# Performance work log

Measured on AMD Instinct MI355X. Metric: run time of the kernel, lower is better.

Reference implementation:

```python
import jax, jax.numpy as jnp
import numpy as np

B, N, C, H = 4, 1024, 1024, 16
HD = C // H


def setup_inputs() -> dict:
    key = jax.random.key(0)
    ks = jax.random.split(key, 9)
    s = 0.02
    return {
        "x": jax.random.normal(ks[0], (B, N, C), dtype=jnp.float32),
        "qkv_w": jax.random.normal(ks[1], (3 * C, C), dtype=jnp.float32) * s,
        "qkv_b": jax.random.normal(ks[2], (3 * C,), dtype=jnp.float32) * s,
        "proj_w": jax.random.normal(ks[3], (C, C), dtype=jnp.float32) * s,
        "proj_b": jax.random.normal(ks[4], (C,), dtype=jnp.float32) * s,
        "wl": jax.random.normal(ks[5], (H, H), dtype=jnp.float32) * s,
        "bl": jax.random.normal(ks[6], (H,), dtype=jnp.float32) * s,
        "ww": jax.random.normal(ks[7], (H, H), dtype=jnp.float32) * s,
        "bw": jax.random.normal(ks[8], (H,), dtype=jnp.float32) * s,
    }


def reference(x, qkv_w, qkv_b, proj_w, proj_b, wl, bl, ww, bw):
    # qkv: torch Linear convention y = x @ W.T + b
    scale = HD ** (-0.5)
    qkv = (jnp.einsum("bnc,oc->bno", x, qkv_w) + qkv_b)
    qkv = qkv.reshape(B, N, 3, H, HD).transpose(2, 0, 3, 1, 4)  # [3,B,H,N,HD]
    q, k, v = qkv[0] * scale, qkv[1], qkv[2]
    attn = jnp.einsum("bhnd,bhmd->bhnm", q, k)  # [B,H,N,N]
    # talking-heads mix before softmax (proj_l over head dim)
    attn = jnp.einsum("bhnm,gh->bgnm", attn, wl) + bl[:, None, None]
    attn = jax.nn.softmax(attn, axis=-1)
    # talking-heads mix after softmax (proj_w over head dim)
    attn = jnp.einsum("bhnm,gh->bgnm", attn, ww) + bw[:, None, None]
    out = jnp.einsum("bhnm,bhmd->bhnd", attn, v)  # [B,H,N,HD]
    out = out.transpose(0, 2, 1, 3).reshape(B, N, C)
    out = jnp.einsum("bnc,oc->bno", out, proj_w) + proj_b
    return out, attn
```

## Files before the change

kernel.cpp:

```cpp
#include <hip/hip_runtime.h>
#include <hip/hip_bf16.h>

typedef unsigned short u16;
typedef __attribute__((ext_vector_type(8))) __bf16 bf16x8;
typedef __attribute__((ext_vector_type(4))) float f32x4;

#define LDSS 40

__device__ __forceinline__ float bf2f(u16 u) {
    unsigned int x = ((unsigned int)u) << 16;
    return __builtin_bit_cast(float, x);
}
__device__ __forceinline__ u16 f2bf(float f) {
    unsigned int x = __builtin_bit_cast(unsigned int, f);
    unsigned int lsb = (x >> 16) & 1u;
    x += 0x7fffu + lsb;
    return (u16)(x >> 16);
}
__device__ __forceinline__ float bf2f_lo(unsigned int u) { return __builtin_bit_cast(float, u << 16); }
__device__ __forceinline__ float bf2f_hi(unsigned int u) { return __builtin_bit_cast(float, u & 0xffff0000u); }

__device__ __forceinline__ void ld8(u16* dst, const u16* src) {
    *(float4*)dst = *(const float4*)src;
}
__device__ __forceinline__ void ld8(u16* dst, const float* src) {
    float4 a = *(const float4*)src;
    float4 b = *(const float4*)(src + 4);
    u16 t[8];
    t[0] = f2bf(a.x); t[1] = f2bf(a.y); t[2] = f2bf(a.z); t[3] = f2bf(a.w);
    t[4] = f2bf(b.x); t[5] = f2bf(b.y); t[6] = f2bf(b.z); t[7] = f2bf(b.w);
    *(float4*)dst = *(float4*)t;
}
__device__ __forceinline__ void stC(u16* p, float v)   { *p = f2bf(v); }
__device__ __forceinline__ void stC(float* p, float v) { *p = v; }

template <typename TA, typename TB, typename TC>
__global__ __launch_bounds__(256)
void gemm_nt(const TA* __restrict__ A, long long sA, int lda,
             const TB* __restrict__ B, long long sB, int ldb,
             TC* __restrict__ C, long long sC, int ldc,
             const float* __restrict__ bias, int K)
{
    __shared__ u16 As[128 * LDSS];
    __shared__ u16 Bs[128 * LDSS];

    const int tid = threadIdx.x;
    const int z = blockIdx.z;
    A += (long long)z * sA;
    B += (long long)z * sB;
    C += (long long)z * sC;
    const int m0 = blockIdx.y * 128;
    const int n0 = blockIdx.x * 128;
    const int wid = tid >> 6;
    const int lane = tid & 63;
    const int wm = (wid >> 1) * 64;
    const int wn = (wid & 1) * 64;
    const int lr = lane & 15;
    const int quad = lane >> 4;

    f32x4 acc[4][4];
#pragma unroll
    for (int i = 0; i < 4; i++)
#pragma unroll
        for (int j = 0; j < 4; j++)
#pragma unroll
            for (int r = 0; r < 4; r++) acc[i][j][r] = 0.f;

    const int srow = tid >> 2;
    const int scol = (tid & 3) * 8;

    for (int k0 = 0; k0 < K; k0 += 32) {
        __syncthreads();
        const TA* ga = A + (long long)(m0 + srow) * lda + k0 + scol;
        ld8(&As[srow * LDSS + scol], ga);
        ld8(&As[(srow + 64) * LDSS + scol], ga + (long long)64 * lda);
        const TB* gb = B + (long long)(n0 + srow) * ldb + k0 + scol;
        ld8(&Bs[srow * LDSS + scol], gb);
        ld8(&Bs[(srow + 64) * LDSS + scol], gb + (long long)64 * ldb);
        __syncthreads();

        bf16x8 af[4], bfr[4];
#pragma unroll
        for (int t = 0; t < 4; t++) {
            af[t]  = *(const bf16x8*)&As[(wm + t * 16 + lr) * LDSS + quad * 8];
            bfr[t] = *(const bf16x8*)&Bs[(wn + t * 16 + lr) * LDSS + quad * 8];
        }
#pragma unroll
        for (int i = 0; i < 4; i++)
#pragma unroll
            for (int j = 0; j < 4; j++)
                acc[i][j] = __builtin_amdgcn_mfma_f32_16x16x32_bf16(af[i], bfr[j], acc[i][j], 0, 0, 0);
    }

#pragma unroll
    for (int j = 0; j < 4; j++) {
        const int col = n0 + wn + j * 16 + lr;
        const float bv = bias ? bias[col] : 0.f;
#pragma unroll
        for (int i = 0; i < 4; i++) {
            const int rbase = m0 + wm + i * 16 + quad * 4;
#pragma unroll
            for (int r = 0; r < 4; r++)
                stC(&C[(long long)(rbase + r) * ldc + col], acc[i][j][r] + bv);
        }
    }
}

__global__ __launch_bounds__(256)
void reorder_qkv(const u16* __restrict__ y, u16* __restrict__ q,
                 u16* __restrict__ k, u16* __restrict__ v)
{
    int t = blockIdx.x * 256 + threadIdx.x;
    int which = t >> 19;
    int r = t & 524287;
    int d8 = r & 7;
    int n = (r >> 3) & 1023;
    int h = (r >> 13) & 15;
    int b = r >> 17;
    const u16* src = y + ((long long)(b * 1024 + n)) * 3072 + which * 1024 + h * 64 + d8 * 8;
    u16* dst = (which == 0 ? q : (which == 1 ? k : v)) +
               (((long long)((b * 16 + h) * 1024 + n)) * 64 + d8 * 8);
    float4 val = *(const float4*)src;
    if (which == 0) {
        u16 tmp[8];
        *(float4*)tmp = val;
#pragma unroll
        for (int i = 0; i < 8; i++) tmp[i] = f2bf(bf2f(tmp[i]) * 0.125f);
        val = *(float4*)tmp;
    }
    *(float4*)dst = val;
}

__global__ __launch_bounds__(256)
void mix_softmax(const u16* __restrict__ S, float* __restrict__ attn_out,
                 u16* __restrict__ attn_bf,
                 const float* __restrict__ wl, const float* __restrict__ bl,
                 const float* __restrict__ ww, const float* __restrict__ bw)
{
    __shared__ float wlT[256];
    __shared__ float wwS[256];
    __shared__ float blS[16];
    __shared__ float bwS[16];
    __shared__ float red[64];
    __shared__ float gsum[16];

    const int tid = threadIdx.x;
    const int lane = tid & 63;
    const int wid = tid >> 6;
    const int b = blockIdx.x >> 10, n = blockIdx.x & 1023;
    const int m0 = tid * 4;

    const long long base = ((long long)(b * 16) * 1024 + n) * 1024 + m0;

    ushort4 pre[4];
#pragma unroll
    for (int h = 0; h < 4; h++)
        pre[h] = *(const ushort4*)(S + base + (long long)h * 1048576);

    wlT[(tid & 15) * 16 + (tid >> 4)] = wl[tid];
    if (tid < 16) { blS[tid] = bl[tid]; bwS[tid] = bw[tid]; }
    __syncthreads();

    f32x4 a[16];
#pragma unroll
    for (int g = 0; g < 16; g++) {
        float bv = blS[g];
        a[g] = (f32x4){bv, bv, bv, bv};
    }

#pragma unroll
    for (int h = 0; h < 16; h++) {
        ushort4 r = pre[h & 3];
        if (h + 4 < 16)
            pre[h & 3] = *(const ushort4*)(S + base + (long long)(h + 4) * 1048576);
        f32x4 sv;
        sv.x = bf2f(r.x); sv.y = bf2f(r.y); sv.z = bf2f(r.z); sv.w = bf2f(r.w);
        float wr[16];
        *(f32x4*)&wr[0]  = *(const f32x4*)&wlT[h * 16];
        *(f32x4*)&wr[4]  = *(const f32x4*)&wlT[h * 16 + 4];
        *(f32x4*)&wr[8]  = *(const f32x4*)&wlT[h * 16 + 8];
        *(f32x4*)&wr[12] = *(const f32x4*)&wlT[h * 16 + 12];
#pragma unroll
        for (int g = 0; g < 16; g++)
            a[g] += sv * wr[g];
    }

#pragma unroll
    for (int g = 0; g < 16; g++) {
        f32x4 p;
        p.x = __expf(a[g].x);
        p.y = __expf(a[g].y);
        p.z = __expf(a[g].z);
        p.w = __expf(a[g].w);
        a[g] = p;
        float vv = (p.x + p.y) + (p.z + p.w);
        for (int off = 32; off; off >>= 1) vv += __shfl_xor(vv, off, 64);
        if (lane == 0) red[wid * 16 + g] = vv;
    }
    __syncthreads();
    if (tid < 16)
        gsum[tid] = (red[tid] + red[16 + tid]) + (red[32 + tid] + red[48 + tid]);
    __syncthreads();
    wwS[tid] = ww[tid] / gsum[tid & 15];
    __syncthreads();

#pragma unroll
    for (int g = 0; g < 16; g++) {
        float wr[16];
        *(f32x4*)&wr[0]  = *(const f32x4*)&wwS[g * 16];
        *(f32x4*)&wr[4]  = *(const f32x4*)&wwS[g * 16 + 4];
        *(f32x4*)&wr[8]  = *(const f32x4*)&wwS[g * 16 + 8];
        *(f32x4*)&wr[12] = *(const f32x4*)&wwS[g * 16 + 12];
        float bv = bwS[g];
        f32x4 o = (f32x4){bv, bv, bv, bv};
#pragma unroll
        for (int h = 0; h < 16; h++)
            o += a[h] * wr[h];
        const long long off = base + (long long)g * 1048576;
        __builtin_nontemporal_store(o, (f32x4*)(attn_out + off));
        ushort4 bo;
        bo.x = f2bf(o.x); bo.y = f2bf(o.y); bo.z = f2bf(o.z); bo.w = f2bf(o.w);
        *(ushort4*)(attn_bf + off) = bo;
    }
}

__global__ __launch_bounds__(256)
void av_gemm(const u16* __restrict__ attn_bf, const u16* __restrict__ v,
             u16* __restrict__ out1)
{
    __shared__ u16 As[64 * LDSS];
    __shared__ u16 Bs[64 * LDSS];

    const int tid = threadIdx.x;
    const int z = blockIdx.z;
    const int b = z >> 4, h = z & 15;
    const int m0 = blockIdx.x * 64;
    const u16* Ab = attn_bf + (long long)z * 1048576;
    const u16* Vb = v + (long long)z * 65536;
    const int wid = tid >> 6;
    const int lane = tid & 63;
    const int lr = lane & 15;
    const int quad = lane >> 4;
    const int wm = wid * 16;

    f32x4 acc[4];
#pragma unroll
    for (int j = 0; j < 4; j++)
#pragma unroll
        for (int r = 0; r < 4; r++) acc[j][r] = 0.f;

    const int srow = tid >> 2;
    const int scol = (tid & 3) * 8;
    const int vrow = tid >> 3;
    const int vdb = (tid & 7) * 8;

    for (int k0 = 0; k0 < 1024; k0 += 32) {
        __syncthreads();
        *(float4*)&As[srow * LDSS + scol] =
            *(const float4*)(Ab + (long long)(m0 + srow) * 1024 + k0 + scol);
        u16 tmp[8];
        *(float4*)tmp = *(const float4*)(Vb + (long long)(k0 + vrow) * 64 + vdb);
#pragma unroll
        for (int j = 0; j < 8; j++) Bs[(vdb + j) * LDSS + vrow] = tmp[j];
        __syncthreads();

        bf16x8 af, bfr[4];
        af = *(const bf16x8*)&As[(wm + lr) * LDSS + quad * 8];
#pragma unroll
        for (int t = 0; t < 4; t++)
            bfr[t] = *(const bf16x8*)&Bs[(t * 16 + lr) * LDSS + quad * 8];
#pragma unroll
        for (int j = 0; j < 4; j++)
            acc[j] = __builtin_amdgcn_mfma_f32_16x16x32_bf16(af, bfr[j], acc[j], 0, 0, 0);
    }

#pragma unroll
    for (int j = 0; j < 4; j++) {
        const int col = h * 64 + j * 16 + lr;
        const int rbase = m0 + wm + quad * 4;
#pragma unroll
        for (int r = 0; r < 4; r++)
            out1[(long long)(b * 1024 + rbase + r) * 1024 + col] = f2bf(acc[j][r]);
    }
}

extern "C" void kernel_launch(void* const* d_in, const int* in_sizes, int n_in,
                              void* d_out, int out_size, void* d_ws, size_t ws_size,
                              hipStream_t stream)
{
    const float* x      = (const float*)d_in[0];
    const float* qkv_w  = (const float*)d_in[1];
    const float* qkv_b  = (const float*)d_in[2];
    const float* proj_w = (const float*)d_in[3];
    const float* proj_b = (const float*)d_in[4];
    const float* wl     = (const float*)d_in[5];
    const float* bl     = (const float*)d_in[6];
    const float* ww     = (const float*)d_in[7];
    const float* bw     = (const float*)d_in[8];

    float* out      = (float*)d_out;
    float* attn_out = out + 4194304;

    u16* ws   = (u16*)d_ws;
    u16* y    = ws;
    u16* q    = ws + 12582912;
    u16* k    = ws + 16777216;
    u16* v    = ws + 20971520;
    u16* s    = ws + 25165824;
    u16* out1 = ws;

    dim3 blk(256);
    gemm_nt<float, float, u16><<<dim3(24, 32, 1), blk, 0, stream>>>(
        x, 0, 1024, qkv_w, 0, 1024, y, 0, 3072, qkv_b, 1024);
    reorder_qkv<<<dim3(6144), blk, 0, stream>>>(y, q, k, v);
    gemm_nt<u16, u16, u16><<<dim3(8, 8, 64), blk, 0, stream>>>(
        q, 65536, 64, k, 65536, 64, s, 1048576, 1024, nullptr, 64);
    mix_softmax<<<dim3(4096), blk, 0, stream>>>(s, attn_out, s, wl, bl, ww, bw);
    av_gemm<<<dim3(16, 1, 64), blk, 0, stream>>>(s, v, out1);
    gemm_nt<u16, float, float><<<dim3(8, 32, 1), blk, 0, stream>>>(
        out1, 0, 1024, proj_w, 0, 1024, out, 0, 1024, proj_b, 1024);
}
```

Measured before the change: 630.8 us.

## Pre-convert fp32 GEMM operands to bf16 and use direct global-to-LDS loads

Adds a bf16 conversion kernel for x, qkv_w and proj_w, so the QKV and output projection GEMMs read bf16 operands. Every bf16 tile load in gemm_nt and av_gemm now uses global_load_lds, which writes straight into LDS without going through registers, and the LDS row stride becomes unpadded 32. The aim is to halve operand bandwidth inside the GEMMs and drop per-tile conversion and register traffic. In exchange it adds three extra kernel launches and conversion passes each call. The unpadded LDS stride may cause bank conflicts on fragment reads.

```diff
diff --git a/kernel.cpp b/kernel.cpp
--- a/kernel.cpp
+++ b/kernel.cpp
@@ -5,7 +5,8 @@
 typedef __attribute__((ext_vector_type(8))) __bf16 bf16x8;
 typedef __attribute__((ext_vector_type(4))) float f32x4;
 
-#define LDSS 40
+template <typename T> struct is16 { static constexpr bool v = false; };
+template <> struct is16<u16> { static constexpr bool v = true; };
 
 __device__ __forceinline__ float bf2f(u16 u) {
     unsigned int x = ((unsigned int)u) << 16;
@@ -17,8 +18,6 @@
     x += 0x7fffu + lsb;
     return (u16)(x >> 16);
 }
-__device__ __forceinline__ float bf2f_lo(unsigned int u) { return __builtin_bit_cast(float, u << 16); }
-__device__ __forceinline__ float bf2f_hi(unsigned int u) { return __builtin_bit_cast(float, u & 0xffff0000u); }
 
 __device__ __forceinline__ void ld8(u16* dst, const u16* src) {
     *(float4*)dst = *(const float4*)src;
@@ -34,6 +33,21 @@
 __device__ __forceinline__ void stC(u16* p, float v)   { *p = f2bf(v); }
 __device__ __forceinline__ void stC(float* p, float v) { *p = v; }
 
+__device__ __forceinline__ void g2l16(const void* g, void* l) {
+    __builtin_amdgcn_global_load_lds(
+        (const __attribute__((address_space(1))) void*)g,
+        (__attribute__((address_space(3))) void*)l, 16, 0, 0);
+}
+
+__global__ __launch_bounds__(256)
+void cvt_bf16(const float* __restrict__ src, u16* __restrict__ dst)
+{
+    long long t = blockIdx.x * 256 + threadIdx.x;
+    u16 tmp[8];
+    ld8(tmp, src + t * 8);
+    *(float4*)(dst + t * 8) = *(float4*)tmp;
+}
+
 template <typename TA, typename TB, typename TC>
 __global__ __launch_bounds__(256)
 void gemm_nt(const TA* __restrict__ A, long long sA, int lda,
@@ -41,8 +55,10 @@
              TC* __restrict__ C, long long sC, int ldc,
              const float* __restrict__ bias, int K)
 {
-    __shared__ u16 As[128 * LDSS];
-    __shared__ u16 Bs[128 * LDSS];
+    constexpr int SA = is16<TA>::v ? 32 : 40;
+    constexpr int SB = is16<TB>::v ? 32 : 40;
+    __shared__ u16 As[128 * SA];
+    __shared__ u16 Bs[128 * SB];
 
     const int tid = threadIdx.x;
     const int z = blockIdx.z;
@@ -72,18 +88,28 @@
     for (int k0 = 0; k0 < K; k0 += 32) {
         __syncthreads();
         const TA* ga = A + (long long)(m0 + srow) * lda + k0 + scol;
-        ld8(&As[srow * LDSS + scol], ga);
-        ld8(&As[(srow + 64) * LDSS + scol], ga + (long long)64 * lda);
+        if constexpr (is16<TA>::v) {
+            g2l16(ga, (char*)As + tid * 16);
+            g2l16(ga + (long long)64 * lda, (char*)As + 4096 + tid * 16);
+        } else {
+            ld8(&As[srow * SA + scol], ga);
+            ld8(&As[(srow + 64) * SA + scol], ga + (long long)64 * lda);
+        }
         const TB* gb = B + (long long)(n0 + srow) * ldb + k0 + scol;
-        ld8(&Bs[srow * LDSS + scol], gb);
-        ld8(&Bs[(srow + 64) * LDSS + scol], gb + (long long)64 * ldb);
+        if constexpr (is16<TB>::v) {
+            g2l16(gb, (char*)Bs + tid * 16);
+            g2l16(gb + (long long)64 * ldb, (char*)Bs + 4096 + tid * 16);
+        } else {
+            ld8(&Bs[srow * SB + scol], gb);
+            ld8(&Bs[(srow + 64) * SB + scol], gb + (long long)64 * ldb);
+        }
         __syncthreads();
 
         bf16x8 af[4], bfr[4];
 #pragma unroll
         for (int t = 0; t < 4; t++) {
-            af[t]  = *(const bf16x8*)&As[(wm + t * 16 + lr) * LDSS + quad * 8];
-            bfr[t] = *(const bf16x8*)&Bs[(wn + t * 16 + lr) * LDSS + quad * 8];
+            af[t]  = *(const bf16x8*)&As[(wm + t * 16 + lr) * SA + quad * 8];
+            bfr[t] = *(const bf16x8*)&Bs[(wn + t * 16 + lr) * SB + quad * 8];
         }
 #pragma unroll
         for (int i = 0; i < 4; i++)
@@ -228,8 +254,8 @@
 void av_gemm(const u16* __restrict__ attn_bf, const u16* __restrict__ v,
              u16* __restrict__ out1)
 {
-    __shared__ u16 As[64 * LDSS];
-    __shared__ u16 Bs[64 * LDSS];
+    __shared__ u16 As[64 * 32];
+    __shared__ u16 Bs[64 * 40];
 
     const int tid = threadIdx.x;
     const int z = blockIdx.z;
@@ -256,19 +282,18 @@
 
     for (int k0 = 0; k0 < 1024; k0 += 32) {
         __syncthreads();
-        *(float4*)&As[srow * LDSS + scol] =
-            *(const float4*)(Ab + (long long)(m0 + srow) * 1024 + k0 + scol);
+        g2l16(Ab + (long long)(m0 + srow) * 1024 + k0 + scol, (char*)As + tid * 16);
         u16 tmp[8];
         *(float4*)tmp = *(const float4*)(Vb + (long long)(k0 + vrow) * 64 + vdb);
 #pragma unroll
-        for (int j = 0; j < 8; j++) Bs[(vdb + j) * LDSS + vrow] = tmp[j];
+        for (int j = 0; j < 8; j++) Bs[(vdb + j) * 40 + vrow] = tmp[j];
         __syncthreads();
 
         bf16x8 af, bfr[4];
-        af = *(const bf16x8*)&As[(wm + lr) * LDSS + quad * 8];
+        af = *(const bf16x8*)&As[(wm + lr) * 32 + quad * 8];
 #pragma unroll
         for (int t = 0; t < 4; t++)
-            bfr[t] = *(const bf16x8*)&Bs[(t * 16 + lr) * LDSS + quad * 8];
+            bfr[t] = *(const bf16x8*)&Bs[(t * 16 + lr) * 40 + quad * 8];
 #pragma unroll
         for (int j = 0; j < 4; j++)
             acc[j] = __builtin_amdgcn_mfma_f32_16x16x32_bf16(af, bfr[j], acc[j], 0, 0, 0);
@@ -309,14 +334,21 @@
     u16* s    = ws + 25165824;
     u16* out1 = ws;
 
+    u16* xb  = s;
+    u16* qwb = s + 4194304;
+    u16* pwb = q;
+
     dim3 blk(256);
-    gemm_nt<float, float, u16><<<dim3(24, 32, 1), blk, 0, stream>>>(
-        x, 0, 1024, qkv_w, 0, 1024, y, 0, 3072, qkv_b, 1024);
+    cvt_bf16<<<dim3(2048), blk, 0, stream>>>(x, xb);
+    cvt_bf16<<<dim3(1536), blk, 0, stream>>>(qkv_w, qwb);
+    gemm_nt<u16, u16, u16><<<dim3(24, 32, 1), blk, 0, stream>>>(
+        xb, 0, 1024, qwb, 0, 1024, y, 0, 3072, qkv_b, 1024);
     reorder_qkv<<<dim3(6144), blk, 0, stream>>>(y, q, k, v);
     gemm_nt<u16, u16, u16><<<dim3(8, 8, 64), blk, 0, stream>>>(
         q, 65536, 64, k, 65536, 64, s, 1048576, 1024, nullptr, 64);
+    cvt_bf16<<<dim3(512), blk, 0, stream>>>(proj_w, pwb);
     mix_softmax<<<dim3(4096), blk, 0, stream>>>(s, attn_out, s, wl, bl, ww, bw);
     av_gemm<<<dim3(16, 1, 64), blk, 0, stream>>>(s, v, out1);
-    gemm_nt<u16, float, float><<<dim3(8, 32, 1), blk, 0, stream>>>(
-        out1, 0, 1024, proj_w, 0, 1024, out, 0, 1024, proj_b, 1024);
-}
+    gemm_nt<u16, u16, float><<<dim3(8, 32, 1), blk, 0, stream>>>(
+        out1, 0, 1024, pwb, 0, 1024, out, 0, 1024, proj_b, 1024);
+}
```

Result: faster. 608.9 us (-3.5%).
